# Kernel tuning notes

Hardware: AMD Instinct MI355X
Metric: run time of the kernel (lower is better)

## Reference

```python
import jax, jax.numpy as jnp
import numpy as np

DIM = 1024
NUM_HEADS = 16
HEAD_DIM = DIM // NUM_HEADS


def _rope_tables(seq_len, dim, dtype):
    # matches llama_rotary_embedding: inv_freq over even indices of head_dim
    inv_freq = 1.0 / (10000.0 ** (jnp.arange(0, dim, 2, dtype=jnp.float32) / dim))
    t = jnp.arange(seq_len, dtype=jnp.float32)
    freqs = jnp.outer(t, inv_freq)  # [S, dim/2]
    return jnp.cos(freqs).astype(dtype), jnp.sin(freqs).astype(dtype)


def _apply_rope(x, cos_emb, sin_emb):
    # x: [B, H, S, hd]; takes interleaved halves, concatenates rotated halves
    x1 = x[..., 0::2]
    x2 = x[..., 1::2]
    return jnp.concatenate((x1 * cos_emb - x2 * sin_emb,
                            x1 * sin_emb + x2 * cos_emb), axis=-1)


def setup_inputs() -> dict:
    key = jax.random.key(0)
    k_x, k_qkv, k_out, k_b = jax.random.split(key, 4)
    B, S, D = 2, 2048, DIM
    x = jax.random.normal(k_x, (B, S, D), dtype=jnp.float32)
    # torch nn.Linear weights are [out_features, in_features]
    w_qkv = jax.random.normal(k_qkv, (3 * D, D), dtype=jnp.float32) * (1.0 / np.sqrt(D))
    w_out = jax.random.normal(k_out, (D, D), dtype=jnp.float32) * (1.0 / np.sqrt(D))
    b_out = jax.random.normal(k_b, (D,), dtype=jnp.float32) * 0.01
    return {"x": x, "w_qkv": w_qkv, "w_out": w_out, "b_out": b_out}


def reference(x, w_qkv, w_out, b_out):
    B, S, D = x.shape
    H, hd = NUM_HEADS, HEAD_DIM
    qkv = jnp.einsum('bsd,ed->bse', x, w_qkv)  # [B, S, 3D]
    q, k, v = jnp.split(qkv, 3, axis=-1)
    # [B, S, D] -> [B, H, S, hd]
    q, k, v = (t.reshape(B, S, H, hd).transpose(0, 2, 1, 3) for t in (q, k, v))
    cos_emb, sin_emb = _rope_tables(S, hd, x.dtype)  # [S, hd/2]
    q = _apply_rope(q, cos_emb, sin_emb)
    k = _apply_rope(k, cos_emb, sin_emb)
    scores = jnp.einsum('bhqd,bhkd->bhqk', q, k) / jnp.sqrt(jnp.asarray(hd, x.dtype))
    attn = jax.nn.softmax(scores, axis=-1)
    out = jnp.einsum('bhqk,bhkd->bhqd', attn, v)
    out = out.transpose(0, 2, 1, 3).reshape(B, S, D)
    return jnp.einsum('bsd,ed->bse', out, w_out) + b_out
```

## Files before the change

kernel.cpp:

```cpp
#include <hip/hip_runtime.h>
#include <math.h>

typedef __bf16 bf16_t;
typedef bf16_t bf16x8 __attribute__((ext_vector_type(8)));
typedef bf16_t bf16x4 __attribute__((ext_vector_type(4)));
typedef short  s16x4  __attribute__((ext_vector_type(4)));
typedef float  f32x4  __attribute__((ext_vector_type(4)));

#define DIM_   1024
#define NHEADS 16
#define HDIM   64
#define SEQ    2048
#define BATCH  2

#define QK_SCALE 0.18033688011112042f

__device__ __forceinline__ s16x4 as_s16x4(bf16x4 v) {
    union { bf16x4 b; s16x4 s; } u; u.b = v; return u.s;
}

__device__ __forceinline__ void gld16(const bf16_t* g, bf16_t* l) {
    __builtin_amdgcn_global_load_lds(
        (const __attribute__((address_space(1))) void*)g,
        (__attribute__((address_space(3))) void*)l, 16, 0, 0);
}

#define XCNT   (4096u * 1024u)
#define WQCNT  (3072u * 1024u)
#define WOCNT  (1024u * 1024u)
__global__ __launch_bounds__(256) void cast3(const float* __restrict__ s0,
                                             const float* __restrict__ s1,
                                             const float* __restrict__ s2,
                                             bf16_t* __restrict__ d0,
                                             bf16_t* __restrict__ d1,
                                             bf16_t* __restrict__ d2) {
    size_t i = ((size_t)blockIdx.x * 256 + threadIdx.x) * 8;
    const float* s; bf16_t* d; size_t off;
    if (i < XCNT)               { s = s0; d = d0; off = i; }
    else if (i < XCNT + WQCNT)  { s = s1; d = d1; off = i - XCNT; }
    else                        { s = s2; d = d2; off = i - XCNT - WQCNT; }
    float4 a = *(const float4*)(s + off);
    float4 b = *(const float4*)(s + off + 4);
    bf16x8 o = { (bf16_t)a.x, (bf16_t)a.y, (bf16_t)a.z, (bf16_t)a.w,
                 (bf16_t)b.x, (bf16_t)b.y, (bf16_t)b.z, (bf16_t)b.w };
    *(bf16x8*)(d + off) = o;
}

template <bool QKV>
__global__ __launch_bounds__(256) void gemm_lds(const bf16_t* __restrict__ A,
                                                const bf16_t* __restrict__ B,
                                                const float* __restrict__ bias,
                                                void* __restrict__ Cout,
                                                bf16_t* __restrict__ vt,
                                                int M, int N, int K) {
    __shared__ __align__(16) bf16_t As[128 * 32];
    __shared__ __align__(16) bf16_t Bs[128 * 32];
    const int tid  = threadIdx.x;
    const int m0   = blockIdx.y * 128;
    const int n0   = blockIdx.x * 128;
    const int w    = tid >> 6;
    const int lane = tid & 63;
    const int m16  = lane & 15;
    const int quad = lane >> 4;
    const int wm   = (w >> 1) * 64;
    const int wn   = (w & 1) * 64;
    const int lrow = lane >> 2;
    const int lcol = (lane & 3) * 8;

    const bf16_t* pa0 = A + (size_t)(m0 + w * 16 + lrow) * K + lcol;
    const bf16_t* pb0 = B + (size_t)(n0 + w * 16 + lrow) * K + lcol;
    bf16_t* lA0 = &As[(w * 16) * 32];
    bf16_t* lA1 = &As[(64 + w * 16) * 32];
    bf16_t* lB0 = &Bs[(w * 16) * 32];
    bf16_t* lB1 = &Bs[(64 + w * 16) * 32];

    f32x4 acc[4][4] = {};

    for (int k0 = 0; k0 < K; k0 += 32) {
        __syncthreads();
        gld16(pa0 + k0, lA0);
        gld16(pa0 + (size_t)64 * K + k0, lA1);
        gld16(pb0 + k0, lB0);
        gld16(pb0 + (size_t)64 * K + k0, lB1);
        __syncthreads();

        bf16x8 af[4], bfr[4];
#pragma unroll
        for (int i = 0; i < 4; ++i)
            af[i] = *(const bf16x8*)(&As[(wm + i * 16 + m16) * 32 + quad * 8]);
#pragma unroll
        for (int j = 0; j < 4; ++j)
            bfr[j] = *(const bf16x8*)(&Bs[(wn + j * 16 + m16) * 32 + quad * 8]);
#pragma unroll
        for (int i = 0; i < 4; ++i)
#pragma unroll
            for (int j = 0; j < 4; ++j)
                acc[i][j] = __builtin_amdgcn_mfma_f32_16x16x32_bf16(af[i], bfr[j], acc[i][j], 0, 0, 0);
    }

    if (QKV && n0 >= 2 * DIM_) {
        const int b      = m0 >> 11;
        const int s_base = (m0 & (SEQ - 1)) + wm;
#pragma unroll
        for (int j = 0; j < 4; ++j) {
            const int cit = wn + j * 16 + m16;
            const int h   = ((n0 - 2 * DIM_) >> 6) + (cit >> 6);
            const int d   = cit & 63;
            bf16_t* vrow = vt + ((size_t)(b * 16 + h) * 64 + d) * SEQ + s_base;
#pragma unroll
            for (int i = 0; i < 4; ++i) {
                bf16x4 ov = { (bf16_t)acc[i][j][0], (bf16_t)acc[i][j][1],
                              (bf16_t)acc[i][j][2], (bf16_t)acc[i][j][3] };
                *(bf16x4*)(vrow + i * 16 + quad * 4) = ov;
            }
        }
    } else if (QKV) {
        bf16_t* C = (bf16_t*)Cout;
#pragma unroll
        for (int i = 0; i < 4; ++i)
#pragma unroll
            for (int j = 0; j < 4; ++j) {
                const int col = n0 + wn + j * 16 + m16;
#pragma unroll
                for (int r = 0; r < 4; ++r)
                    C[(size_t)(m0 + wm + i * 16 + quad * 4 + r) * N + col] = (bf16_t)acc[i][j][r];
            }
    } else {
        float* C = (float*)Cout;
#pragma unroll
        for (int j = 0; j < 4; ++j) {
            const int col = n0 + wn + j * 16 + m16;
            const float bv = bias[col];
#pragma unroll
            for (int i = 0; i < 4; ++i)
#pragma unroll
                for (int r = 0; r < 4; ++r)
                    C[(size_t)(m0 + wm + i * 16 + quad * 4 + r) * N + col] = acc[i][j][r] + bv;
        }
    }
}

__global__ __launch_bounds__(256) void gemm_out64(const bf16_t* __restrict__ A,
                                                  const bf16_t* __restrict__ B,
                                                  const float* __restrict__ bias,
                                                  float* __restrict__ C,
                                                  int M, int N, int K) {
    __shared__ __align__(16) bf16_t As[128 * 32];
    __shared__ __align__(16) bf16_t Bs[64 * 32];
    const int tid  = threadIdx.x;
    const int m0   = blockIdx.y * 128;
    const int n0   = blockIdx.x * 64;
    const int w    = tid >> 6;
    const int lane = tid & 63;
    const int m16  = lane & 15;
    const int quad = lane >> 4;
    const int wm   = (w >> 1) * 64;
    const int wn   = (w & 1) * 32;
    const int lrow = lane >> 2;
    const int lcol = (lane & 3) * 8;

    const bf16_t* pa0 = A + (size_t)(m0 + w * 16 + lrow) * K + lcol;
    const bf16_t* pb0 = B + (size_t)(n0 + w * 16 + lrow) * K + lcol;
    bf16_t* lA0 = &As[(w * 16) * 32];
    bf16_t* lA1 = &As[(64 + w * 16) * 32];
    bf16_t* lB0 = &Bs[(w * 16) * 32];

    f32x4 acc[4][2] = {};

    for (int k0 = 0; k0 < K; k0 += 32) {
        __syncthreads();
        gld16(pa0 + k0, lA0);
        gld16(pa0 + (size_t)64 * K + k0, lA1);
        gld16(pb0 + k0, lB0);
        __syncthreads();

        bf16x8 af[4], bfr[2];
#pragma unroll
        for (int i = 0; i < 4; ++i)
            af[i] = *(const bf16x8*)(&As[(wm + i * 16 + m16) * 32 + quad * 8]);
#pragma unroll
        for (int j = 0; j < 2; ++j)
            bfr[j] = *(const bf16x8*)(&Bs[(wn + j * 16 + m16) * 32 + quad * 8]);
#pragma unroll
        for (int i = 0; i < 4; ++i)
#pragma unroll
            for (int j = 0; j < 2; ++j)
                acc[i][j] = __builtin_amdgcn_mfma_f32_16x16x32_bf16(af[i], bfr[j], acc[i][j], 0, 0, 0);
    }

#pragma unroll
    for (int j = 0; j < 2; ++j) {
        const int col = n0 + wn + j * 16 + m16;
        const float bv = bias[col];
#pragma unroll
        for (int i = 0; i < 4; ++i)
#pragma unroll
            for (int r = 0; r < 4; ++r)
                C[(size_t)(m0 + wm + i * 16 + quad * 4 + r) * N + col] = acc[i][j][r] + bv;
    }
}

__global__ __launch_bounds__(256) void rope_bf16(bf16_t* __restrict__ qkv) {
    __shared__ float ctab[8][32];
    __shared__ float stab[8][32];
    const int tid = threadIdx.x;
    const int sl  = tid >> 5, j = tid & 31;
    const int s   = (int)((blockIdx.x * 8 + sl) & (SEQ - 1));
    const float freq = exp2f(-0.41524101186092029f * (float)j);
    float sn, cs;
    sincosf((float)s * freq, &sn, &cs);
    ctab[sl][j] = cs;
    stab[sl][j] = sn;
    __syncthreads();

    const int gid   = blockIdx.x * 256 + tid;
    const int m     = gid >> 5;
    const int rr    = gid & 31;
    const int which = rr >> 4;
    const int hh    = rr & 15;
    const float osc = (which == 0) ? QK_SCALE : 1.0f;

    bf16_t* p = qkv + (size_t)m * (3 * DIM_) + which * DIM_ + hh * HDIM;
    union { bf16_t e[64]; bf16x8 v[8]; } X, O;
#pragma unroll
    for (int i = 0; i < 8; ++i) X.v[i] = *(const bf16x8*)(p + i * 8);
#pragma unroll
    for (int t = 0; t < 32; ++t) {
        const float x1 = (float)X.e[2 * t];
        const float x2 = (float)X.e[2 * t + 1];
        const float c  = ctab[sl][t];
        const float s2 = stab[sl][t];
        O.e[t]      = (bf16_t)((x1 * c - x2 * s2) * osc);
        O.e[32 + t] = (bf16_t)((x1 * s2 + x2 * c) * osc);
    }
#pragma unroll
    for (int i = 0; i < 8; ++i) *(bf16x8*)(p + i * 8) = O.v[i];
}

__global__ __launch_bounds__(256) void attn_mfma(const bf16_t* __restrict__ qkv,
                                                 const bf16_t* __restrict__ vt,
                                                 bf16_t* __restrict__ out) {
    __shared__ __align__(16) char smem[18432];
    bf16_t* Ks   = (bf16_t*)smem;
    bf16_t* Vt   = (bf16_t*)(smem + 9216);
    float*  Ored = (float*)smem;
    float*  Lred = (float*)(smem + 16640);

    const int tid  = threadIdx.x;
    const int w    = tid >> 6;
    const int lane = tid & 63;
    const int m16  = lane & 15;
    const int quad = lane >> 4;
    const int bh   = blockIdx.y;
    const int b    = bh >> 4;
    const int hh   = bh & 15;
    const int q0   = blockIdx.x * 64;

    const size_t rs = 3 * DIM_;
    const bf16_t* qbase = qkv + (size_t)(b * SEQ) * rs + hh * HDIM;
    const bf16_t* kbase = qbase + DIM_;
    const bf16_t* vtg   = vt + (size_t)bh * 64 * SEQ;

    bf16x8 qf[4][2];
#pragma unroll
    for (int n = 0; n < 4; ++n)
#pragma unroll
        for (int kt = 0; kt < 2; ++kt)
            qf[n][kt] = *(const bf16x8*)(qbase + (size_t)(q0 + n * 16 + m16) * rs + kt * 32 + quad * 8);

    f32x4 o[4][4] = {};
    float lp[4] = {};

    const int srow = tid >> 3;
    const int sc8  = (tid & 7) * 8;

    bf16x8 kreg[2], vreg[2];
#pragma unroll
    for (int p = 0; p < 2; ++p) {
        const int row = srow + p * 32;
        kreg[p] = *(const bf16x8*)(kbase + (size_t)row * rs + sc8);
        vreg[p] = *(const bf16x8*)(vtg + (size_t)row * SEQ + sc8);
    }

    for (int t = 0; t < 32; ++t) {
        __syncthreads();
#pragma unroll
        for (int p = 0; p < 2; ++p) {
            const int row = srow + p * 32;
            *(bf16x8*)(&Ks[row * 72 + sc8]) = kreg[p];
            *(bf16x8*)(&Vt[row * 72 + sc8]) = vreg[p];
        }
        __syncthreads();

        if (t < 31) {
            const size_t k0n = (size_t)(t + 1) * 64;
#pragma unroll
            for (int p = 0; p < 2; ++p) {
                const int row = srow + p * 32;
                kreg[p] = *(const bf16x8*)(kbase + (k0n + row) * rs + sc8);
                vreg[p] = *(const bf16x8*)(vtg + (size_t)row * SEQ + k0n + sc8);
            }
        }

        bf16x8 ak0 = *(const bf16x8*)(&Ks[(w * 16 + m16) * 72 + 0 * 32 + quad * 8]);
        bf16x8 ak1 = *(const bf16x8*)(&Ks[(w * 16 + m16) * 72 + 1 * 32 + quad * 8]);
        bf16x4 va[4];
#pragma unroll
        for (int ds = 0; ds < 4; ++ds)
            va[ds] = *(const bf16x4*)(&Vt[(ds * 16 + m16) * 72 + w * 16 + quad * 4]);

        s16x4 pb[4];
#pragma unroll
        for (int n = 0; n < 4; ++n) {
            f32x4 c = {};
            c = __builtin_amdgcn_mfma_f32_16x16x32_bf16(ak0, qf[n][0], c, 0, 0, 0);
            c = __builtin_amdgcn_mfma_f32_16x16x32_bf16(ak1, qf[n][1], c, 0, 0, 0);
            bf16x4 pv;
#pragma unroll
            for (int r = 0; r < 4; ++r) {
                const float p = __builtin_amdgcn_exp2f(c[r]);
                lp[n] += p;
                pv[r] = (bf16_t)p;
            }
            pb[n] = as_s16x4(pv);
        }

#pragma unroll
        for (int ds = 0; ds < 4; ++ds)
#pragma unroll
            for (int n = 0; n < 4; ++n)
                o[ds][n] = __builtin_amdgcn_mfma_f32_16x16x16bf16_1k(as_s16x4(va[ds]), pb[n], o[ds][n], 0, 0, 0);
    }

#pragma unroll
    for (int n = 0; n < 4; ++n) {
        lp[n] += __shfl_xor(lp[n], 16);
        lp[n] += __shfl_xor(lp[n], 32);
    }
    __syncthreads();
    if (quad == 0) {
#pragma unroll
        for (int n = 0; n < 4; ++n) Lred[w * 64 + n * 16 + m16] = lp[n];
    }
    __syncthreads();
    const float linv = 1.0f / (Lred[lane] + Lred[64 + lane] + Lred[128 + lane] + Lred[192 + lane]);

    const size_t obase = (size_t)(b * SEQ + q0 + lane) * DIM_ + hh * HDIM;
#pragma unroll
    for (int p = 0; p < 4; ++p) {
        __syncthreads();
#pragma unroll
        for (int n = 0; n < 4; ++n)
#pragma unroll
            for (int r = 0; r < 4; ++r)
                Ored[w * 1040 + (quad * 4 + r) * 65 + n * 16 + m16] = o[p][n][r];
        __syncthreads();
        if (w == p) {
            union { bf16_t e[16]; bf16x8 v[2]; } ob;
#pragma unroll
            for (int d = 0; d < 16; ++d) {
                const float v = Ored[d * 65 + lane] + Ored[1040 + d * 65 + lane] +
                                Ored[2080 + d * 65 + lane] + Ored[3120 + d * 65 + lane];
                ob.e[d] = (bf16_t)(v * linv);
            }
            *(bf16x8*)(out + obase + p * 16)     = ob.v[0];
            *(bf16x8*)(out + obase + p * 16 + 8) = ob.v[1];
        }
    }
}

extern "C" void kernel_launch(void* const* d_in, const int* in_sizes, int n_in,
                              void* d_out, int out_size, void* d_ws, size_t ws_size,
                              hipStream_t stream) {
    const float* x     = (const float*)d_in[0];
    const float* w_qkv = (const float*)d_in[1];
    const float* w_out = (const float*)d_in[2];
    const float* b_out = (const float*)d_in[3];
    float* out = (float*)d_out;

    const int M = BATCH * SEQ;

    bf16_t* qkv_b  = (bf16_t*)d_ws;
    bf16_t* attn_b = qkv_b + (size_t)M * 3 * DIM_;
    bf16_t* vt_b   = attn_b + (size_t)M * DIM_;
    bf16_t* xb     = vt_b + (size_t)BATCH * NHEADS * HDIM * SEQ;
    bf16_t* wqkvb  = xb + (size_t)M * DIM_;
    bf16_t* woutb  = wqkvb + (size_t)3 * DIM_ * DIM_;

    cast3<<<(XCNT + WQCNT + WOCNT) / (256 * 8), 256, 0, stream>>>(
        x, w_qkv, w_out, xb, wqkvb, woutb);

    gemm_lds<true><<<dim3(3 * DIM_ / 128, M / 128), 256, 0, stream>>>(
        xb, wqkvb, nullptr, qkv_b, vt_b, M, 3 * DIM_, DIM_);

    rope_bf16<<<(M * 2 * NHEADS) / 256, 256, 0, stream>>>(qkv_b);

    attn_mfma<<<dim3(SEQ / 64, BATCH * NHEADS), 256, 0, stream>>>(qkv_b, vt_b, attn_b);

    gemm_out64<<<dim3(DIM_ / 64, M / 128), 256, 0, stream>>>(
        attn_b, woutb, b_out, out, M, DIM_, DIM_);
}
```

Measured before the change: 221.8 us.

## Double-buffer K/V tiles in LDS to halve barriers per attention step

Splits the shared K and V tile storage into two ping-pong buffers. The next tile is written into the alternate buffer after the current compute, so each step needs one barrier instead of two, and the loop is unrolled by two. It also raises wave priority around the PV MFMA block with s_setprio. LDS use roughly doubles, which may reduce the number of resident blocks per CU.

```diff
diff --git a/kernel.cpp b/kernel.cpp
--- a/kernel.cpp
+++ b/kernel.cpp
@@ -240,11 +240,13 @@
 __global__ __launch_bounds__(256) void attn_mfma(const bf16_t* __restrict__ qkv,
                                                  const bf16_t* __restrict__ vt,
                                                  bf16_t* __restrict__ out) {
-    __shared__ __align__(16) char smem[18432];
-    bf16_t* Ks   = (bf16_t*)smem;
-    bf16_t* Vt   = (bf16_t*)(smem + 9216);
+    __shared__ __align__(16) char smem[37888];
+    bf16_t* Ks0  = (bf16_t*)smem;
+    bf16_t* Vt0  = (bf16_t*)(smem + 9216);
+    bf16_t* Ks1  = (bf16_t*)(smem + 18432);
+    bf16_t* Vt1  = (bf16_t*)(smem + 27648);
     float*  Ored = (float*)smem;
-    float*  Lred = (float*)(smem + 16640);
+    float*  Lred = (float*)(smem + 36864);
 
     const int tid  = threadIdx.x;
     const int w    = tid >> 6;
@@ -275,69 +277,84 @@
     const int sc8  = (tid & 7) * 8;
 
     bf16x8 kreg[2], vreg[2];
+
 #pragma unroll
     for (int p = 0; p < 2; ++p) {
         const int row = srow + p * 32;
         kreg[p] = *(const bf16x8*)(kbase + (size_t)row * rs + sc8);
         vreg[p] = *(const bf16x8*)(vtg + (size_t)row * SEQ + sc8);
     }
-
-    for (int t = 0; t < 32; ++t) {
-        __syncthreads();
-#pragma unroll
-        for (int p = 0; p < 2; ++p) {
-            const int row = srow + p * 32;
-            *(bf16x8*)(&Ks[row * 72 + sc8]) = kreg[p];
-            *(bf16x8*)(&Vt[row * 72 + sc8]) = vreg[p];
-        }
-        __syncthreads();
-
-        if (t < 31) {
-            const size_t k0n = (size_t)(t + 1) * 64;
-#pragma unroll
-            for (int p = 0; p < 2; ++p) {
-                const int row = srow + p * 32;
-                kreg[p] = *(const bf16x8*)(kbase + (k0n + row) * rs + sc8);
-                vreg[p] = *(const bf16x8*)(vtg + (size_t)row * SEQ + k0n + sc8);
-            }
-        }
-
-        bf16x8 ak0 = *(const bf16x8*)(&Ks[(w * 16 + m16) * 72 + 0 * 32 + quad * 8]);
-        bf16x8 ak1 = *(const bf16x8*)(&Ks[(w * 16 + m16) * 72 + 1 * 32 + quad * 8]);
-        bf16x4 va[4];
-#pragma unroll
-        for (int ds = 0; ds < 4; ++ds)
-            va[ds] = *(const bf16x4*)(&Vt[(ds * 16 + m16) * 72 + w * 16 + quad * 4]);
-
-        s16x4 pb[4];
-#pragma unroll
-        for (int n = 0; n < 4; ++n) {
-            f32x4 c = {};
-            c = __builtin_amdgcn_mfma_f32_16x16x32_bf16(ak0, qf[n][0], c, 0, 0, 0);
-            c = __builtin_amdgcn_mfma_f32_16x16x32_bf16(ak1, qf[n][1], c, 0, 0, 0);
-            bf16x4 pv;
-#pragma unroll
-            for (int r = 0; r < 4; ++r) {
-                const float p = __builtin_amdgcn_exp2f(c[r]);
-                lp[n] += p;
-                pv[r] = (bf16_t)p;
-            }
-            pb[n] = as_s16x4(pv);
-        }
-
-#pragma unroll
-        for (int ds = 0; ds < 4; ++ds)
-#pragma unroll
-            for (int n = 0; n < 4; ++n)
-                o[ds][n] = __builtin_amdgcn_mfma_f32_16x16x16bf16_1k(as_s16x4(va[ds]), pb[n], o[ds][n], 0, 0, 0);
-    }
+#pragma unroll
+    for (int p = 0; p < 2; ++p) {
+        const int row = srow + p * 32;
+        *(bf16x8*)(&Ks0[row * 72 + sc8]) = kreg[p];
+        *(bf16x8*)(&Vt0[row * 72 + sc8]) = vreg[p];
+    }
+    __syncthreads();
+
+#define ATTN_BODY(T, KS, VS, KSN, VSN)                                             \
+    do {                                                                           \
+        const int tt = (T);                                                        \
+        if (tt < 31) {                                                             \
+            const size_t k0n = (size_t)(tt + 1) * 64;                              \
+            _Pragma("unroll")                                                      \
+            for (int p = 0; p < 2; ++p) {                                          \
+                const int row = srow + p * 32;                                     \
+                kreg[p] = *(const bf16x8*)(kbase + (k0n + row) * rs + sc8);        \
+                vreg[p] = *(const bf16x8*)(vtg + (size_t)row * SEQ + k0n + sc8);   \
+            }                                                                      \
+        }                                                                          \
+        bf16x8 ak0 = *(const bf16x8*)(&KS[(w * 16 + m16) * 72 + 0 * 32 + quad * 8]); \
+        bf16x8 ak1 = *(const bf16x8*)(&KS[(w * 16 + m16) * 72 + 1 * 32 + quad * 8]); \
+        bf16x4 va[4];                                                              \
+        _Pragma("unroll")                                                          \
+        for (int ds = 0; ds < 4; ++ds)                                             \
+            va[ds] = *(const bf16x4*)(&VS[(ds * 16 + m16) * 72 + w * 16 + quad * 4]); \
+        s16x4 pb[4];                                                               \
+        _Pragma("unroll")                                                          \
+        for (int n = 0; n < 4; ++n) {                                              \
+            f32x4 c = {};                                                          \
+            c = __builtin_amdgcn_mfma_f32_16x16x32_bf16(ak0, qf[n][0], c, 0, 0, 0); \
+            c = __builtin_amdgcn_mfma_f32_16x16x32_bf16(ak1, qf[n][1], c, 0, 0, 0); \
+            bf16x4 pv;                                                             \
+            _Pragma("unroll")                                                      \
+            for (int r = 0; r < 4; ++r) {                                          \
+                const float pp = __builtin_amdgcn_exp2f(c[r]);                     \
+                lp[n] += pp;                                                       \
+                pv[r] = (bf16_t)pp;                                                \
+            }                                                                      \
+            pb[n] = as_s16x4(pv);                                                  \
+        }                                                                          \
+        __builtin_amdgcn_s_setprio(1);                                             \
+        _Pragma("unroll")                                                          \
+        for (int ds = 0; ds < 4; ++ds)                                             \
+            _Pragma("unroll")                                                      \
+            for (int n = 0; n < 4; ++n)                                            \
+                o[ds][n] = __builtin_amdgcn_mfma_f32_16x16x16bf16_1k(               \
+                    as_s16x4(va[ds]), pb[n], o[ds][n], 0, 0, 0);                   \
+        __builtin_amdgcn_s_setprio(0);                                             \
+        if (tt < 31) {                                                             \
+            _Pragma("unroll")                                                      \
+            for (int p = 0; p < 2; ++p) {                                          \
+                const int row = srow + p * 32;                                     \
+                *(bf16x8*)(&KSN[row * 72 + sc8]) = kreg[p];                        \
+                *(bf16x8*)(&VSN[row * 72 + sc8]) = vreg[p];                        \
+            }                                                                      \
+        }                                                                          \
+        __syncthreads();                                                           \
+    } while (0)
+
+    for (int t = 0; t < 32; t += 2) {
+        ATTN_BODY(t,     Ks0, Vt0, Ks1, Vt1);
+        ATTN_BODY(t + 1, Ks1, Vt1, Ks0, Vt0);
+    }
+#undef ATTN_BODY
 
 #pragma unroll
     for (int n = 0; n < 4; ++n) {
         lp[n] += __shfl_xor(lp[n], 16);
         lp[n] += __shfl_xor(lp[n], 32);
     }
-    __syncthreads();
     if (quad == 0) {
 #pragma unroll
         for (int n = 0; n < 4; ++n) Lred[w * 64 + n * 16 + m16] = lp[n];
```

New measurement: 215.6 us. 2.8% less time.
